# Performance work log

Hardware: AMD Instinct MI355X
Metric: run time of the kernel (lower is better)

## Reference

```python
import jax, jax.numpy as jnp
import numpy as np

N = 50000   # nodes per type (d and t)
E = 500000  # edges per relation
D = 128     # in = out features
NEG_SLOPE = 0.2


def setup_inputs() -> dict:
    key = jax.random.key(0)
    ks = jax.random.split(key, 24)
    s = 1.0 / np.sqrt(D)
    inp = {
        'x_d': jax.random.normal(ks[0], (N, D), jnp.float32),
        'x_t': jax.random.normal(ks[1], (N, D), jnp.float32),
        'W_dd': jax.random.normal(ks[2], (D, D), jnp.float32) * s,
        'W_tt': jax.random.normal(ks[3], (D, D), jnp.float32) * s,
        'W_dt': jax.random.normal(ks[4], (D, D), jnp.float32) * s,
        'al_dd': jax.random.normal(ks[5], (D,), jnp.float32) * s,
        'ar_dd': jax.random.normal(ks[6], (D,), jnp.float32) * s,
        'al_tt': jax.random.normal(ks[7], (D,), jnp.float32) * s,
        'ar_tt': jax.random.normal(ks[8], (D,), jnp.float32) * s,
        'al_dt': jax.random.normal(ks[9], (D,), jnp.float32) * s,
        'ar_dt': jax.random.normal(ks[10], (D,), jnp.float32) * s,
        'b_dd': jnp.zeros((D,), jnp.float32),
        'b_tt': jnp.zeros((D,), jnp.float32),
        'b_dt': jnp.zeros((D,), jnp.float32),
        'src_dd': jax.random.randint(ks[11], (E,), 0, N),
        'dst_dd': jax.random.randint(ks[12], (E,), 0, N),
        'src_tt': jax.random.randint(ks[13], (E,), 0, N),
        'dst_tt': jax.random.randint(ks[14], (E,), 0, N),
        'src_dt': jax.random.randint(ks[15], (E,), 0, N),
        'dst_dt': jax.random.randint(ks[16], (E,), 0, N),
        'src_td': jax.random.randint(ks[17], (E,), 0, N),
        'dst_td': jax.random.randint(ks[18], (E,), 0, N),
    }
    return inp


def _gat(x_src, x_dst, W, al, ar, b, src, dst, n_dst):
    """DGL GATConv (num_heads=1, no dropout, eval): gather -> edge attn ->
    per-destination segment softmax -> scatter-weighted aggregation + bias."""
    fs = x_src @ W                      # [Ns, D]
    fd = x_dst @ W                      # [Nd, D]
    el = fs @ al                        # [Ns]
    er = fd @ ar                        # [Nd]
    e = jax.nn.leaky_relu(el[src] + er[dst], NEG_SLOPE)   # [E]
    m = jax.ops.segment_max(e, dst, num_segments=n_dst)
    m = jnp.where(jnp.isfinite(m), m, jnp.float32(0))      # isolated dst nodes
    ex = jnp.exp(e - m[dst])
    ssum = jax.ops.segment_sum(ex, dst, num_segments=n_dst)
    alpha = ex / ssum[dst]              # [E]
    out = jax.ops.segment_sum(alpha[:, None] * fs[src], dst, num_segments=n_dst)
    return out + b


def reference(x_d, x_t, W_dd, W_tt, W_dt,
              al_dd, ar_dd, al_tt, ar_tt, al_dt, ar_dt,
              b_dd, b_tt, b_dt,
              src_dd, dst_dd, src_tt, dst_tt,
              src_dt, dst_dt, src_td, dst_td):
    # HeteroGraphConv with aggregate='sum'; 'dt' and 'td' share parameters.
    h_d = (_gat(x_d, x_d, W_dd, al_dd, ar_dd, b_dd, src_dd, dst_dd, N)
           + _gat(x_t, x_d, W_dt, al_dt, ar_dt, b_dt, src_td, dst_td, N))
    h_t = (_gat(x_t, x_t, W_tt, al_tt, ar_tt, b_tt, src_tt, dst_tt, N)
           + _gat(x_d, x_t, W_dt, al_dt, ar_dt, b_dt, src_dt, dst_dt, N))
    return jnp.stack([h_d, h_t])        # [2, N, D]
```

## Files before the change

kernel.cpp:

```cpp
#include <hip/hip_runtime.h>
#include <hip/hip_bf16.h>
#include <hip/hip_fp16.h>
#include <math.h>

#define DD 128
#define NEG_SLOPE 0.2f
#define CAP_B 2048
#define BSHIFT 7
#define MAXNB 512
#define SCAT_BLKS 64

typedef __attribute__((ext_vector_type(8))) short bf16x8;
typedef __attribute__((ext_vector_type(4))) float f32x4;
typedef __attribute__((ext_vector_type(8))) unsigned short u16x8;

__device__ __forceinline__ short f2bf(float f) {
    __hip_bfloat16 h = __float2bfloat16(f);
    return __builtin_bit_cast(short, h);
}
__device__ __forceinline__ float bf2f(unsigned short u) {
    return __uint_as_float(((unsigned)u) << 16);
}
__device__ __forceinline__ unsigned short f2h(float f) {
    return __builtin_bit_cast(unsigned short, __float2half(f));
}
__device__ __forceinline__ float h2f(unsigned short u) {
    return __half2float(__builtin_bit_cast(__half, u));
}
__device__ __forceinline__ float lrexp(float e) {
    e = (e > 0.f) ? e : NEG_SLOPE * e;
    return __expf(e);
}

__global__ __launch_bounds__(256) void pack_init_k(
    const float* __restrict__ W0, const float* __restrict__ W1,
    const float* __restrict__ W2,
    unsigned short* __restrict__ P0, unsigned short* __restrict__ P1,
    unsigned short* __restrict__ P2, int* __restrict__ cursor)
{
    if (blockIdx.x >= 24) {
        const int i = (blockIdx.x - 24) * 256 + threadIdx.x;
        if (i < 4 * MAXNB) cursor[i] = (i & (MAXNB - 1)) * CAP_B;
        return;
    }
    const int t = blockIdx.x * 256 + threadIdx.x;
    const int m = t >> 11;
    const int r = t & 2047;
    const float* W = (m == 0) ? W0 : (m == 1) ? W1 : W2;
    unsigned short* P = (m == 0) ? P0 : (m == 1) ? P1 : P2;
    const int lane = r & 63;
    const int tile = r >> 6;
    const int ks = tile >> 3, ct = tile & 7;
    const int col = ct * 16 + (lane & 15);
    const int k0 = ks * 32 + (lane >> 4) * 8;
#pragma unroll
    for (int j = 0; j < 8; ++j)
        P[(size_t)r * 8 + j] = (unsigned short)f2bf(W[(size_t)(k0 + j) * DD + col]);
}

__device__ __forceinline__ void epi_store(
    f32x4 acc[8], const float* __restrict__ al, const float* __restrict__ ar,
    unsigned short* __restrict__ fb, float* __restrict__ el,
    float* __restrict__ er, int r0, int lane, int nrows)
{
    float pl[4] = {0.f, 0.f, 0.f, 0.f};
    float pr[4] = {0.f, 0.f, 0.f, 0.f};
#pragma unroll
    for (int ct = 0; ct < 8; ++ct) {
        const float alc = al[ct * 16 + (lane & 15)];
        const float arc = ar[ct * 16 + (lane & 15)];
#pragma unroll
        for (int g = 0; g < 4; ++g) {
            pl[g] = fmaf(acc[ct][g], alc, pl[g]);
            pr[g] = fmaf(acc[ct][g], arc, pr[g]);
        }
    }
#pragma unroll
    for (int o = 1; o < 16; o <<= 1) {
#pragma unroll
        for (int g = 0; g < 4; ++g) {
            pl[g] += __shfl_xor(pl[g], o, 16);
            pr[g] += __shfl_xor(pr[g], o, 16);
        }
    }
    if ((lane & 15) == 0) {
#pragma unroll
        for (int g = 0; g < 4; ++g) {
            const int r = r0 + (lane >> 4) * 4 + g;
            if (r < nrows) { el[r] = pl[g]; er[r] = pr[g]; }
        }
    }
#pragma unroll
    for (int g = 0; g < 4; ++g) {
        const int r = r0 + (lane >> 4) * 4 + g;
        if (r < nrows) {
            unsigned short* fp = fb + (size_t)r * DD + (lane & 15);
#pragma unroll
            for (int ct = 0; ct < 8; ++ct)
                fp[ct * 16] = (unsigned short)f2bf(acc[ct][g]);
        }
    }
}

struct Prep3Args {
    const float* x[4];
    const unsigned short* Wp[4];
    const float* al[4]; const float* ar[4];
    unsigned short* fb[4]; float* el[4]; float* er[4];
    const int* src[4]; const int* dst[4];
    int* cursor; unsigned* ebuf;
    int n, nE, nb;
};

__global__ __launch_bounds__(512) void prep3_k(Prep3Args P)
{
    __shared__ unsigned short wlds[2048 * 8];

    const int v = blockIdx.y;
    if (v < 4) {
        const uint4* wsrc = (const uint4*)P.Wp[v];
        uint4* wdst = (uint4*)wlds;
#pragma unroll
        for (int i = 0; i < 4; ++i)
            wdst[threadIdx.x + i * 512] = wsrc[threadIdx.x + i * 512];
        __syncthreads();

        const int lane = threadIdx.x & 63;
        const int wave = threadIdx.x >> 6;
        const int r0 = (blockIdx.x * 8 + wave) * 16;
        if (r0 >= P.n) return;

        const int arow = r0 + (lane & 15);
        const int arow_c = (arow < P.n) ? arow : (P.n - 1);
        const int kbase = (lane >> 4) * 8;
        const float* x = P.x[v];

        f32x4 acc[8];
#pragma unroll
        for (int ct = 0; ct < 8; ++ct) acc[ct] = (f32x4)(0.f);

#pragma unroll
        for (int ks = 0; ks < 4; ++ks) {
            const float* xp = x + (size_t)arow_c * DD + ks * 32 + kbase;
            const float4 a0 = ((const float4*)xp)[0];
            const float4 a1 = ((const float4*)xp)[1];
            bf16x8 af;
            af[0] = f2bf(a0.x); af[1] = f2bf(a0.y); af[2] = f2bf(a0.z); af[3] = f2bf(a0.w);
            af[4] = f2bf(a1.x); af[5] = f2bf(a1.y); af[6] = f2bf(a1.z); af[7] = f2bf(a1.w);
#pragma unroll
            for (int ct = 0; ct < 8; ++ct) {
                const bf16x8 w = *((const bf16x8*)(wlds + ((size_t)(ks * 8 + ct) * 64 + lane) * 8));
                acc[ct] = __builtin_amdgcn_mfma_f32_16x16x32_bf16(af, w, acc[ct], 0, 0, 0);
            }
        }
        epi_store(acc, P.al[v], P.ar[v], P.fb[v], P.el[v], P.er[v], r0, lane, P.n);
        return;
    }

    const int sb = blockIdx.x;
    if (sb >= 4 * SCAT_BLKS) return;
    int* cnt_s  = (int*)wlds;
    int* base_s = ((int*)wlds) + MAXNB;
    const int rel = sb >> 6;
    const int blk = sb & (SCAT_BLKS - 1);
    const int* src = P.src[rel];
    const int* dst = P.dst[rel];
    int* cur = P.cursor + (size_t)rel * MAXNB;
    unsigned* eb = P.ebuf + (size_t)rel * P.nb * CAP_B;

    const int t = threadIdx.x;
    const int ch = (P.nE + SCAT_BLKS - 1) / SCAT_BLKS;
    const int i0 = blk * ch;
    const int i1 = (i0 + ch < P.nE) ? (i0 + ch) : P.nE;

    for (int i = t; i < MAXNB; i += 512) cnt_s[i] = 0;
    __syncthreads();
    for (int i = i0 + t; i < i1; i += 512)
        atomicAdd(&cnt_s[dst[i] >> BSHIFT], 1);
    __syncthreads();
    for (int b = t; b < P.nb; b += 512) {
        const int c = cnt_s[b];
        base_s[b] = c ? atomicAdd(cur + b, c) : 0;
        cnt_s[b] = 0;
    }
    __syncthreads();
    for (int i = i0 + t; i < i1; i += 512) {
        const int dv = dst[i];
        const int b = dv >> BSHIFT;
        const int p = base_s[b] + atomicAdd(&cnt_s[b], 1);
        eb[p] = ((unsigned)(dv & ((1 << BSHIFT) - 1)) << 16) | (unsigned)src[i];
    }
}

struct SortArgs {
    const float* el[4]; const float* er[4];
};

__global__ __launch_bounds__(256) void sort_alpha_k(
    const unsigned* __restrict__ ebuf, const int* __restrict__ cursor,
    SortArgs S, unsigned* __restrict__ cs32, int* __restrict__ rstart,
    int* __restrict__ rdeg, int n, int nb)
{
    const int b = blockIdx.x, rel = blockIdx.y, t = threadIdx.x;
    int cnt = cursor[(size_t)rel * MAXNB + b] - b * CAP_B;
    cnt = (cnt < 0) ? 0 : (cnt > CAP_B) ? CAP_B : cnt;

    __shared__ unsigned buf[CAP_B];
    __shared__ unsigned out32[CAP_B];
    __shared__ int hist[128], off[128], cnt2[128], excl[128];
    __shared__ float ssum[128];
    __shared__ int total_s;

    const unsigned* ebr = ebuf + ((size_t)rel * nb + b) * CAP_B;
    for (int i = t; i < cnt; i += 256) buf[i] = ebr[i];
    if (t < 128) { hist[t] = 0; cnt2[t] = 0; ssum[t] = 0.f; }
    __syncthreads();
    for (int i = t; i < cnt; i += 256) atomicAdd(&hist[buf[i] >> 16], 1);
    __syncthreads();
    if (t < 128) off[t] = (hist[t] + 3) & ~3;
    __syncthreads();
    for (int o = 1; o < 128; o <<= 1) {
        const int v = (t < 128 && t >= o) ? off[t - o] : 0;
        __syncthreads();
        if (t < 128) off[t] += v;
        __syncthreads();
    }
    if (t < 128) {
        const int pc = (hist[t] + 3) & ~3;
        excl[t] = off[t] - pc;
        const int d = b * 128 + t;
        if (d < n) {
            rstart[(size_t)rel * n + d] = b * CAP_B + excl[t];
            rdeg[(size_t)rel * n + d] = pc;
        }
        for (int i = excl[t] + hist[t]; i < off[t]; ++i) out32[i] = 0u;
    }
    if (t == 127) total_s = off[127];
    __syncthreads();

    const float* el = S.el[rel];
    const float* er = S.er[rel];
    for (int i = t; i < cnt; i += 256) {
        const unsigned v = buf[i];
        const int local = v >> 16;
        const int s = v & 0xffffu;
        const float ex = lrexp(el[s] + er[b * 128 + local]);
        atomicAdd(&ssum[local], ex);
        const int p = excl[local] + atomicAdd(&cnt2[local], 1);
        out32[p] = (unsigned)s | ((unsigned)f2h(ex) << 16);
    }
    __syncthreads();
    if (t < 128 && hist[t] > 0) {
        const float inv = 1.f / ssum[t];
        const int e0 = excl[t], e1 = excl[t] + hist[t];
        for (int i = e0; i < e1; ++i) {
            const unsigned v = out32[i];
            const float alpha = h2f((unsigned short)(v >> 16)) * inv;
            out32[i] = (v & 0xffffu) | ((unsigned)f2h(alpha) << 16);
        }
    }
    __syncthreads();
    unsigned* cs = cs32 + ((size_t)rel * nb + b) * CAP_B;
    const int total = total_s;
    for (int i = t; i < total; i += 256) cs[i] = out32[i];
}

struct AggArgs {
    const int* rs[4]; const int* rd[4];
    const unsigned* cs[4];
    const unsigned short* fb[4];
    const float* bA[2]; const float* bB[2];
    float* out[2];
    int n;
};

__device__ __forceinline__ void agg16p(
    const int* __restrict__ rs, const int* __restrict__ rd,
    const unsigned* __restrict__ cs, const unsigned short* __restrict__ fb,
    int d, int lane, float4& o0, float4& o1)
{
    const int cnt = rd[d];
    if (cnt == 0) return;
    const unsigned* csp = cs + rs[d];
    for (int k = 0; k < cnt; k += 4) {
        unsigned pv[4];
#pragma unroll
        for (int j = 0; j < 4; ++j) pv[j] = csp[k + j];
        u16x8 v[4];
#pragma unroll
        for (int j = 0; j < 4; ++j)
            v[j] = ((const u16x8*)(fb + (size_t)(pv[j] & 0xffffu) * DD))[lane];
#pragma unroll
        for (int j = 0; j < 4; ++j) {
            const float a = h2f((unsigned short)(pv[j] >> 16));
            o0.x = fmaf(a, bf2f(v[j][0]), o0.x);
            o0.y = fmaf(a, bf2f(v[j][1]), o0.y);
            o0.z = fmaf(a, bf2f(v[j][2]), o0.z);
            o0.w = fmaf(a, bf2f(v[j][3]), o0.w);
            o1.x = fmaf(a, bf2f(v[j][4]), o1.x);
            o1.y = fmaf(a, bf2f(v[j][5]), o1.y);
            o1.z = fmaf(a, bf2f(v[j][6]), o1.z);
            o1.w = fmaf(a, bf2f(v[j][7]), o1.w);
        }
    }
}

__global__ __launch_bounds__(256) void gat_aggregate_f(AggArgs A)
{
    const int lane = threadIdx.x & 15;
    const int grp  = threadIdx.x >> 4;
    const int gid = blockIdx.x * 16 + grp;
    if (gid >= 2 * A.n) return;
    const int ty = (gid >= A.n) ? 1 : 0;
    const int d = gid - ty * A.n;
    const int sl1 = ty ? 1 : 0;
    const int sl2 = ty ? 2 : 3;

    const float4 ba0 = ((const float4*)A.bA[ty])[lane * 2];
    const float4 ba1 = ((const float4*)A.bA[ty])[lane * 2 + 1];
    const float4 bb0 = ((const float4*)A.bB[ty])[lane * 2];
    const float4 bb1 = ((const float4*)A.bB[ty])[lane * 2 + 1];
    float4 o0 = make_float4(ba0.x + bb0.x, ba0.y + bb0.y, ba0.z + bb0.z, ba0.w + bb0.w);
    float4 o1 = make_float4(ba1.x + bb1.x, ba1.y + bb1.y, ba1.z + bb1.z, ba1.w + bb1.w);

    agg16p(A.rs[sl1], A.rd[sl1], A.cs[sl1], A.fb[sl1], d, lane, o0, o1);
    agg16p(A.rs[sl2], A.rd[sl2], A.cs[sl2], A.fb[sl2], d, lane, o0, o1);

    float4* op = (float4*)(A.out[ty] + (size_t)d * DD);
    op[lane * 2] = o0;
    op[lane * 2 + 1] = o1;
}

extern "C" void kernel_launch(void* const* d_in, const int* in_sizes, int n_in,
                              void* d_out, int out_size, void* d_ws, size_t ws_size,
                              hipStream_t stream)
{
    const float* x_d  = (const float*)d_in[0];
    const float* x_t  = (const float*)d_in[1];
    const float* W_dd = (const float*)d_in[2];
    const float* W_tt = (const float*)d_in[3];
    const float* W_dt = (const float*)d_in[4];
    const float* al_dd = (const float*)d_in[5];
    const float* ar_dd = (const float*)d_in[6];
    const float* al_tt = (const float*)d_in[7];
    const float* ar_tt = (const float*)d_in[8];
    const float* al_dt = (const float*)d_in[9];
    const float* ar_dt = (const float*)d_in[10];
    const float* b_dd  = (const float*)d_in[11];
    const float* b_tt  = (const float*)d_in[12];
    const float* b_dt  = (const float*)d_in[13];
    const int* src_dd = (const int*)d_in[14];
    const int* dst_dd = (const int*)d_in[15];
    const int* src_tt = (const int*)d_in[16];
    const int* dst_tt = (const int*)d_in[17];
    const int* src_dt = (const int*)d_in[18];
    const int* dst_dt = (const int*)d_in[19];
    const int* src_td = (const int*)d_in[20];
    const int* dst_td = (const int*)d_in[21];

    const int n  = in_sizes[0] / DD;
    const int nE = in_sizes[14];
    const int nb = (n + 127) >> BSHIFT;

    float* ws = (float*)d_ws;
    size_t off = 0;
    unsigned short* fb_dd   = (unsigned short*)(ws + off); off += (size_t)n * DD / 2;
    unsigned short* fb_tt   = (unsigned short*)(ws + off); off += (size_t)n * DD / 2;
    unsigned short* fb_dt_d = (unsigned short*)(ws + off); off += (size_t)n * DD / 2;
    unsigned short* fb_dt_t = (unsigned short*)(ws + off); off += (size_t)n * DD / 2;
    unsigned* ebuf = (unsigned*)(ws + off); off += (size_t)4 * nb * CAP_B;
    unsigned* cs32 = (unsigned*)(ws + off); off += (size_t)4 * nb * CAP_B;
    float* el_dd   = ws + off; off += n;
    float* er_dd   = ws + off; off += n;
    float* el_tt   = ws + off; off += n;
    float* er_tt   = ws + off; off += n;
    float* el_dt_d = ws + off; off += n;
    float* er_dt_d = ws + off; off += n;
    float* el_dt_t = ws + off; off += n;
    float* er_dt_t = ws + off; off += n;
    int* rstart = (int*)(ws + off); off += (size_t)4 * n;
    int* rdeg   = (int*)(ws + off); off += (size_t)4 * n;
    int* cursor = (int*)(ws + off); off += (size_t)4 * MAXNB;
    unsigned short* Wp_dd = (unsigned short*)(ws + off); off += 2048 * 8 / 2;
    unsigned short* Wp_tt = (unsigned short*)(ws + off); off += 2048 * 8 / 2;
    unsigned short* Wp_dt = (unsigned short*)(ws + off); off += 2048 * 8 / 2;

    if (ws_size < off * sizeof(float)) return;

    pack_init_k<<<32, 256, 0, stream>>>(W_dd, W_tt, W_dt, Wp_dd, Wp_tt, Wp_dt, cursor);

    Prep3Args P;
    P.x[0] = x_d; P.x[1] = x_t; P.x[2] = x_d; P.x[3] = x_t;
    P.Wp[0] = Wp_dd; P.Wp[1] = Wp_tt; P.Wp[2] = Wp_dt; P.Wp[3] = Wp_dt;
    P.al[0] = al_dd; P.al[1] = al_tt; P.al[2] = al_dt; P.al[3] = al_dt;
    P.ar[0] = ar_dd; P.ar[1] = ar_tt; P.ar[2] = ar_dt; P.ar[3] = ar_dt;
    P.fb[0] = fb_dd; P.fb[1] = fb_tt; P.fb[2] = fb_dt_d; P.fb[3] = fb_dt_t;
    P.el[0] = el_dd; P.el[1] = el_tt; P.el[2] = el_dt_d; P.el[3] = el_dt_t;
    P.er[0] = er_dd; P.er[1] = er_tt; P.er[2] = er_dt_d; P.er[3] = er_dt_t;
    P.src[0] = src_dd; P.dst[0] = dst_dd;
    P.src[1] = src_tt; P.dst[1] = dst_tt;
    P.src[2] = src_dt; P.dst[2] = dst_dt;
    P.src[3] = src_td; P.dst[3] = dst_td;
    P.cursor = cursor; P.ebuf = ebuf;
    P.n = n; P.nE = nE; P.nb = nb;

    int gx = (n + 127) / 128;
    if (gx < 4 * SCAT_BLKS) gx = 4 * SCAT_BLKS;
    dim3 pgrid(gx, 5);
    prep3_k<<<pgrid, 512, 0, stream>>>(P);

    SortArgs S;
    S.el[0] = el_dd;   S.er[0] = er_dd;
    S.el[1] = el_tt;   S.er[1] = er_tt;
    S.el[2] = el_dt_d; S.er[2] = er_dt_t;
    S.el[3] = el_dt_t; S.er[3] = er_dt_d;
    dim3 bgrid(nb, 4);
    sort_alpha_k<<<bgrid, 256, 0, stream>>>(ebuf, cursor, S, cs32, rstart, rdeg, n, nb);

    const size_t reg = (size_t)nb * CAP_B;
    AggArgs A;
    A.rs[0] = rstart + 0 * (size_t)n; A.rd[0] = rdeg + 0 * (size_t)n;
    A.rs[1] = rstart + 1 * (size_t)n; A.rd[1] = rdeg + 1 * (size_t)n;
    A.rs[2] = rstart + 2 * (size_t)n; A.rd[2] = rdeg + 2 * (size_t)n;
    A.rs[3] = rstart + 3 * (size_t)n; A.rd[3] = rdeg + 3 * (size_t)n;
    A.cs[0] = cs32 + 0 * reg; A.cs[1] = cs32 + 1 * reg;
    A.cs[2] = cs32 + 2 * reg; A.cs[3] = cs32 + 3 * reg;
    A.fb[0] = fb_dd; A.fb[1] = fb_tt;
    A.fb[2] = fb_dt_d;
    A.fb[3] = fb_dt_t;
    A.bA[0] = b_dd; A.bB[0] = b_dt;
    A.bA[1] = b_tt; A.bB[1] = b_dt;
    A.out[0] = (float*)d_out;
    A.out[1] = (float*)d_out + (size_t)n * DD;
    A.n = n;

    const int aggrid = (2 * n + 15) / 16;
    gat_aggregate_f<<<aggrid, 256, 0, stream>>>(A);
}
```

Measured before the change: 150.4 us.

## Use persistent grid for projection GEMM and fewer scatter blocks per relation

The projection part of the combined prep kernel now launches a fixed 96 blocks per weight slot, each looping over row tiles, instead of one block per 128-row tile. This loads the packed weight matrix into LDS once per block rather than once per tile. The edge-binning part drops from 64 to 24 blocks per relation, so each block handles a larger edge chunk and fewer global cursor atomics occur per bucket. The trade-off is less parallelism, so fewer waves are available to hide memory latency in both phases.

```diff
diff --git a/kernel.cpp b/kernel.cpp
--- a/kernel.cpp
+++ b/kernel.cpp
@@ -8,7 +8,8 @@
 #define CAP_B 2048
 #define BSHIFT 7
 #define MAXNB 512
-#define SCAT_BLKS 64
+#define TBLK 96
+#define NSCAT 24
 
 typedef __attribute__((ext_vector_type(8))) short bf16x8;
 typedef __attribute__((ext_vector_type(4))) float f32x4;
@@ -102,17 +103,17 @@
     }
 }
 
-struct Prep3Args {
+struct Prep4Args {
     const float* x[4];
     const unsigned short* Wp[4];
     const float* al[4]; const float* ar[4];
     unsigned short* fb[4]; float* el[4]; float* er[4];
     const int* src[4]; const int* dst[4];
     int* cursor; unsigned* ebuf;
-    int n, nE, nb;
+    int n, nE, nb, ntiles;
 };
 
-__global__ __launch_bounds__(512) void prep3_k(Prep3Args P)
+__global__ __launch_bounds__(512) void prep4_k(Prep4Args P)
 {
     __shared__ unsigned short wlds[2048 * 8];
 
@@ -127,49 +128,51 @@
 
         const int lane = threadIdx.x & 63;
         const int wave = threadIdx.x >> 6;
-        const int r0 = (blockIdx.x * 8 + wave) * 16;
-        if (r0 >= P.n) return;
-
-        const int arow = r0 + (lane & 15);
-        const int arow_c = (arow < P.n) ? arow : (P.n - 1);
         const int kbase = (lane >> 4) * 8;
         const float* x = P.x[v];
 
-        f32x4 acc[8];
-#pragma unroll
-        for (int ct = 0; ct < 8; ++ct) acc[ct] = (f32x4)(0.f);
-
-#pragma unroll
-        for (int ks = 0; ks < 4; ++ks) {
-            const float* xp = x + (size_t)arow_c * DD + ks * 32 + kbase;
-            const float4 a0 = ((const float4*)xp)[0];
-            const float4 a1 = ((const float4*)xp)[1];
-            bf16x8 af;
-            af[0] = f2bf(a0.x); af[1] = f2bf(a0.y); af[2] = f2bf(a0.z); af[3] = f2bf(a0.w);
-            af[4] = f2bf(a1.x); af[5] = f2bf(a1.y); af[6] = f2bf(a1.z); af[7] = f2bf(a1.w);
-#pragma unroll
-            for (int ct = 0; ct < 8; ++ct) {
-                const bf16x8 w = *((const bf16x8*)(wlds + ((size_t)(ks * 8 + ct) * 64 + lane) * 8));
-                acc[ct] = __builtin_amdgcn_mfma_f32_16x16x32_bf16(af, w, acc[ct], 0, 0, 0);
+        for (int tile = blockIdx.x; tile < P.ntiles; tile += TBLK) {
+            const int r0 = (tile * 8 + wave) * 16;
+            if (r0 >= P.n) continue;
+            const int arow = r0 + (lane & 15);
+            const int arow_c = (arow < P.n) ? arow : (P.n - 1);
+
+            f32x4 acc[8];
+#pragma unroll
+            for (int ct = 0; ct < 8; ++ct) acc[ct] = (f32x4)(0.f);
+
+#pragma unroll
+            for (int ks = 0; ks < 4; ++ks) {
+                const float* xp = x + (size_t)arow_c * DD + ks * 32 + kbase;
+                const float4 a0 = ((const float4*)xp)[0];
+                const float4 a1 = ((const float4*)xp)[1];
+                bf16x8 af;
+                af[0] = f2bf(a0.x); af[1] = f2bf(a0.y); af[2] = f2bf(a0.z); af[3] = f2bf(a0.w);
+                af[4] = f2bf(a1.x); af[5] = f2bf(a1.y); af[6] = f2bf(a1.z); af[7] = f2bf(a1.w);
+#pragma unroll
+                for (int ct = 0; ct < 8; ++ct) {
+                    const bf16x8 w = *((const bf16x8*)(wlds + ((size_t)(ks * 8 + ct) * 64 + lane) * 8));
+                    acc[ct] = __builtin_amdgcn_mfma_f32_16x16x32_bf16(af, w, acc[ct], 0, 0, 0);
+                }
             }
-        }
-        epi_store(acc, P.al[v], P.ar[v], P.fb[v], P.el[v], P.er[v], r0, lane, P.n);
+            epi_store(acc, P.al[v], P.ar[v], P.fb[v], P.el[v], P.er[v], r0, lane, P.n);
+        }
         return;
     }
 
     const int sb = blockIdx.x;
-    if (sb >= 4 * SCAT_BLKS) return;
+    if (sb >= 4 * NSCAT) return;
     int* cnt_s  = (int*)wlds;
     int* base_s = ((int*)wlds) + MAXNB;
-    const int rel = sb >> 6;
-    const int blk = sb & (SCAT_BLKS - 1);
+    const int rel = sb / NSCAT;
+    const int blk = sb - rel * NSCAT;
     const int* src = P.src[rel];
     const int* dst = P.dst[rel];
     int* cur = P.cursor + (size_t)rel * MAXNB;
     unsigned* eb = P.ebuf + (size_t)rel * P.nb * CAP_B;
 
     const int t = threadIdx.x;
-    const int ch = (P.nE + SCAT_BLKS - 1) / SCAT_BLKS;
+    const int ch = (P.nE + NSCAT - 1) / NSCAT;
     const int i0 = blk * ch;
     const int i1 = (i0 + ch < P.nE) ? (i0 + ch) : P.nE;
 
@@ -361,6 +364,7 @@
     const int n  = in_sizes[0] / DD;
     const int nE = in_sizes[14];
     const int nb = (n + 127) >> BSHIFT;
+    const int ntiles = (n + 127) / 128;
 
     float* ws = (float*)d_ws;
     size_t off = 0;
@@ -389,7 +393,7 @@
 
     pack_init_k<<<32, 256, 0, stream>>>(W_dd, W_tt, W_dt, Wp_dd, Wp_tt, Wp_dt, cursor);
 
-    Prep3Args P;
+    Prep4Args P;
     P.x[0] = x_d; P.x[1] = x_t; P.x[2] = x_d; P.x[3] = x_t;
     P.Wp[0] = Wp_dd; P.Wp[1] = Wp_tt; P.Wp[2] = Wp_dt; P.Wp[3] = Wp_dt;
     P.al[0] = al_dd; P.al[1] = al_tt; P.al[2] = al_dt; P.al[3] = al_dt;
@@ -402,12 +406,10 @@
     P.src[2] = src_dt; P.dst[2] = dst_dt;
     P.src[3] = src_td; P.dst[3] = dst_td;
     P.cursor = cursor; P.ebuf = ebuf;
-    P.n = n; P.nE = nE; P.nb = nb;
-
-    int gx = (n + 127) / 128;
-    if (gx < 4 * SCAT_BLKS) gx = 4 * SCAT_BLKS;
-    dim3 pgrid(gx, 5);
-    prep3_k<<<pgrid, 512, 0, stream>>>(P);
+    P.n = n; P.nE = nE; P.nb = nb; P.ntiles = ntiles;
+
+    dim3 pgrid(TBLK, 5);
+    prep4_k<<<pgrid, 512, 0, stream>>>(P);
 
     SortArgs S;
     S.el[0] = el_dd;   S.er[0] = er_dd;
```

After: 155.1 us. 3.2% more time.

## Store projected features in permuted column layout for vectorized writes and gathers

Applied to the files above, without the earlier changes.

The GEMM epilogue now writes each row's 8 bf16 values per lane as a single 16-byte vector, storing features in a column-permuted layout. The aggregation kernel compensates by writing outputs with a strided per-lane pattern, and the two biases are pre-summed into a permuted vector in the init kernel. Prep blocks past the row range also exit before loading the weights into LDS. This swaps many scattered 2-byte feature stores for wide ones, at the cost of less coalesced fp32 output stores.

```diff
diff --git a/kernel.cpp b/kernel.cpp
--- a/kernel.cpp
+++ b/kernel.cpp
@@ -32,15 +32,25 @@
     return __expf(e);
 }
 
+__device__ __forceinline__ int permcol(int cp) { return (cp & 7) * 16 + (cp >> 3); }
+
 __global__ __launch_bounds__(256) void pack_init_k(
     const float* __restrict__ W0, const float* __restrict__ W1,
     const float* __restrict__ W2,
     unsigned short* __restrict__ P0, unsigned short* __restrict__ P1,
-    unsigned short* __restrict__ P2, int* __restrict__ cursor)
+    unsigned short* __restrict__ P2, int* __restrict__ cursor,
+    const float* __restrict__ b_dd, const float* __restrict__ b_tt,
+    const float* __restrict__ b_dt, float* __restrict__ pb0,
+    float* __restrict__ pb1)
 {
     if (blockIdx.x >= 24) {
         const int i = (blockIdx.x - 24) * 256 + threadIdx.x;
         if (i < 4 * MAXNB) cursor[i] = (i & (MAXNB - 1)) * CAP_B;
+        if (blockIdx.x == 24) {
+            const int t = threadIdx.x;
+            if (t < 128) pb0[t] = b_dd[permcol(t)] + b_dt[permcol(t)];
+            else         pb1[t - 128] = b_tt[permcol(t - 128)] + b_dt[permcol(t - 128)];
+        }
         return;
     }
     const int t = blockIdx.x * 256 + threadIdx.x;
@@ -94,15 +104,16 @@
     for (int g = 0; g < 4; ++g) {
         const int r = r0 + (lane >> 4) * 4 + g;
         if (r < nrows) {
-            unsigned short* fp = fb + (size_t)r * DD + (lane & 15);
+            u16x8 v;
 #pragma unroll
             for (int ct = 0; ct < 8; ++ct)
-                fp[ct * 16] = (unsigned short)f2bf(acc[ct][g]);
-        }
-    }
-}
-
-struct Prep3Args {
+                v[ct] = (unsigned short)f2bf(acc[ct][g]);
+            *((u16x8*)(fb + (size_t)r * DD + (lane & 15) * 8)) = v;
+        }
+    }
+}
+
+struct Prep5Args {
     const float* x[4];
     const unsigned short* Wp[4];
     const float* al[4]; const float* ar[4];
@@ -112,12 +123,17 @@
     int n, nE, nb;
 };
 
-__global__ __launch_bounds__(512) void prep3_k(Prep3Args P)
+__global__ __launch_bounds__(512) void prep5_k(Prep5Args P)
 {
     __shared__ unsigned short wlds[2048 * 8];
 
     const int v = blockIdx.y;
     if (v < 4) {
+        const int lane = threadIdx.x & 63;
+        const int wave = threadIdx.x >> 6;
+        const int r0 = (blockIdx.x * 8 + wave) * 16;
+        if (blockIdx.x * 128 >= P.n) return;
+
         const uint4* wsrc = (const uint4*)P.Wp[v];
         uint4* wdst = (uint4*)wlds;
 #pragma unroll
@@ -125,11 +141,7 @@
             wdst[threadIdx.x + i * 512] = wsrc[threadIdx.x + i * 512];
         __syncthreads();
 
-        const int lane = threadIdx.x & 63;
-        const int wave = threadIdx.x >> 6;
-        const int r0 = (blockIdx.x * 8 + wave) * 16;
         if (r0 >= P.n) return;
-
         const int arow = r0 + (lane & 15);
         const int arow_c = (arow < P.n) ? arow : (P.n - 1);
         const int kbase = (lane >> 4) * 8;
@@ -269,7 +281,7 @@
     const int* rs[4]; const int* rd[4];
     const unsigned* cs[4];
     const unsigned short* fb[4];
-    const float* bA[2]; const float* bB[2];
+    const float* pb[2];
     float* out[2];
     int n;
 };
@@ -316,19 +328,15 @@
     const int sl1 = ty ? 1 : 0;
     const int sl2 = ty ? 2 : 3;
 
-    const float4 ba0 = ((const float4*)A.bA[ty])[lane * 2];
-    const float4 ba1 = ((const float4*)A.bA[ty])[lane * 2 + 1];
-    const float4 bb0 = ((const float4*)A.bB[ty])[lane * 2];
-    const float4 bb1 = ((const float4*)A.bB[ty])[lane * 2 + 1];
-    float4 o0 = make_float4(ba0.x + bb0.x, ba0.y + bb0.y, ba0.z + bb0.z, ba0.w + bb0.w);
-    float4 o1 = make_float4(ba1.x + bb1.x, ba1.y + bb1.y, ba1.z + bb1.z, ba1.w + bb1.w);
+    float4 o0 = ((const float4*)A.pb[ty])[lane * 2];
+    float4 o1 = ((const float4*)A.pb[ty])[lane * 2 + 1];
 
     agg16p(A.rs[sl1], A.rd[sl1], A.cs[sl1], A.fb[sl1], d, lane, o0, o1);
     agg16p(A.rs[sl2], A.rd[sl2], A.cs[sl2], A.fb[sl2], d, lane, o0, o1);
 
-    float4* op = (float4*)(A.out[ty] + (size_t)d * DD);
-    op[lane * 2] = o0;
-    op[lane * 2 + 1] = o1;
+    float* op = A.out[ty] + (size_t)d * DD + lane;
+    op[0]   = o0.x; op[16]  = o0.y; op[32]  = o0.z; op[48]  = o0.w;
+    op[64]  = o1.x; op[80]  = o1.y; op[96]  = o1.z; op[112] = o1.w;
 }
 
 extern "C" void kernel_launch(void* const* d_in, const int* in_sizes, int n_in,
@@ -384,12 +392,15 @@
     unsigned short* Wp_dd = (unsigned short*)(ws + off); off += 2048 * 8 / 2;
     unsigned short* Wp_tt = (unsigned short*)(ws + off); off += 2048 * 8 / 2;
     unsigned short* Wp_dt = (unsigned short*)(ws + off); off += 2048 * 8 / 2;
+    float* pb0 = ws + off; off += DD;
+    float* pb1 = ws + off; off += DD;
 
     if (ws_size < off * sizeof(float)) return;
 
-    pack_init_k<<<32, 256, 0, stream>>>(W_dd, W_tt, W_dt, Wp_dd, Wp_tt, Wp_dt, cursor);
-
-    Prep3Args P;
+    pack_init_k<<<32, 256, 0, stream>>>(W_dd, W_tt, W_dt, Wp_dd, Wp_tt, Wp_dt,
+                                        cursor, b_dd, b_tt, b_dt, pb0, pb1);
+
+    Prep5Args P;
     P.x[0] = x_d; P.x[1] = x_t; P.x[2] = x_d; P.x[3] = x_t;
     P.Wp[0] = Wp_dd; P.Wp[1] = Wp_tt; P.Wp[2] = Wp_dt; P.Wp[3] = Wp_dt;
     P.al[0] = al_dd; P.al[1] = al_tt; P.al[2] = al_dt; P.al[3] = al_dt;
@@ -407,7 +418,7 @@
     int gx = (n + 127) / 128;
     if (gx < 4 * SCAT_BLKS) gx = 4 * SCAT_BLKS;
     dim3 pgrid(gx, 5);
-    prep3_k<<<pgrid, 512, 0, stream>>>(P);
+    prep5_k<<<pgrid, 512, 0, stream>>>(P);
 
     SortArgs S;
     S.el[0] = el_dd;   S.er[0] = er_dd;
@@ -428,8 +439,7 @@
     A.fb[0] = fb_dd; A.fb[1] = fb_tt;
     A.fb[2] = fb_dt_d;
     A.fb[3] = fb_dt_t;
-    A.bA[0] = b_dd; A.bB[0] = b_dt;
-    A.bA[1] = b_tt; A.bB[1] = b_dt;
+    A.pb[0] = pb0; A.pb[1] = pb1;
     A.out[0] = (float*)d_out;
     A.out[1] = (float*)d_out + (size_t)n * DD;
     A.n = n;
```

After: 148.9 us. Within noise of the previous version (-0.9%).
